# Kernel tuning notes

Hardware: AMD Instinct MI355X
Metric: run time of the kernel (lower is better)

## Reference

```python
import jax, jax.numpy as jnp
import numpy as np

EPSILON = 1e-09
BETA = 0.75  # original code clamps negative-sample sigmoid to min=BETA (reproduced faithfully)
B, D, V, NUM_SAMPLES = 262144, 256, 50000, 5


def setup_inputs() -> dict:
    key = jax.random.key(0)
    k1, k2, k3, k4 = jax.random.split(key, 4)
    context = jax.random.normal(k1, (B, D), dtype=jnp.float32)
    target = jax.random.normal(k2, (B, D), dtype=jnp.float32)
    emb = jax.random.normal(k3, (V, D), dtype=jnp.float32)
    neg_idx = jax.random.randint(k4, (NUM_SAMPLES,), 0, V)  # precomputed unigram-table draws
    return {"context": context, "target": target, "emb": emb, "neg_idx": neg_idx}


def reference(context, target, emb, neg_idx):
    # positive term: log(sigmoid(<c, t>).clamp(min=EPSILON))
    dots = jnp.sum(context * target, axis=-1)  # [B]
    log_targets = jnp.log(jnp.clip(jax.nn.sigmoid(dots), EPSILON, None))
    # negative samples: NUM_SAMPLES embedding rows shared across the batch
    samples = emb[neg_idx]  # [S, D]
    neg_dots = -jnp.einsum('bd,sd->bs', context, samples)  # [B, S]
    log_samples = jnp.log(jnp.clip(jax.nn.sigmoid(neg_dots), BETA, None)).sum(axis=-1)  # [B]
    return jnp.sum(log_targets + log_samples)
```

## Files before the change

kernel.cpp:

```cpp
#include <hip/hip_runtime.h>

static constexpr int B_ROWS  = 262144;
static constexpr int D       = 256;
static constexpr int NSAMP   = 5;
static constexpr int BLOCK   = 256;
static constexpr int NBLOCKS = 4096;
static constexpr int WPB     = BLOCK / 64;
static constexpr int GPW     = 16;

static constexpr float NEG_LN_EPS  = 20.723265836946411f;
static constexpr float NEG_LN_BETA = 0.28768207245178085f;

__device__ __forceinline__ float dot4(const float4 a, const float4 b) {
    return a.x * b.x + a.y * b.y + a.z * b.z + a.w * b.w;
}

__global__ __launch_bounds__(BLOCK) void sgns_main(
    const float* __restrict__ ctx, const float* __restrict__ tgt,
    const float* __restrict__ emb, const int* __restrict__ neg_idx,
    float* __restrict__ partials)
{
    __shared__ float smp[NSAMP][D];
    for (int i = threadIdx.x; i < NSAMP * D; i += BLOCK) {
        const int s = i >> 8, c = i & (D - 1);
        smp[s][c] = emb[(size_t)neg_idx[s] * D + c];
    }
    __syncthreads();

    const int lane = threadIdx.x & 63;
    const int wid  = threadIdx.x >> 6;
    const int sub  = lane & 3;
    const int grp  = lane >> 2;
    const int gwave  = blockIdx.x * WPB + wid;
    const int nwaves = NBLOCKS * WPB;

    float acc = 0.0f;
    for (int rbase = gwave * GPW; rbase < B_ROWS; rbase += nwaves * GPW) {
        const float* cp = ctx + (size_t)(rbase + grp) * D + sub * 4;
        const float* tp = tgt + (size_t)(rbase + grp) * D + sub * 4;

        float d0 = 0.f, d1 = 0.f, d2 = 0.f, d3 = 0.f, d4 = 0.f, d5 = 0.f;
#pragma unroll 8
        for (int m = 0; m < 16; ++m) {
            const float4 c4 = *reinterpret_cast<const float4*>(cp + m * 16);
            const float4 t4 = *reinterpret_cast<const float4*>(tp + m * 16);
            const int sc = m * 16 + sub * 4;
            const float4 s0 = *reinterpret_cast<const float4*>(&smp[0][sc]);
            const float4 s1 = *reinterpret_cast<const float4*>(&smp[1][sc]);
            const float4 s2 = *reinterpret_cast<const float4*>(&smp[2][sc]);
            const float4 s3 = *reinterpret_cast<const float4*>(&smp[3][sc]);
            const float4 s4 = *reinterpret_cast<const float4*>(&smp[4][sc]);
            d0 += dot4(c4, t4);
            d1 += dot4(c4, s0);
            d2 += dot4(c4, s1);
            d3 += dot4(c4, s2);
            d4 += dot4(c4, s3);
            d5 += dot4(c4, s4);
        }

        d0 += __shfl_xor(d0, 1, 64); d0 += __shfl_xor(d0, 2, 64);
        d1 += __shfl_xor(d1, 1, 64); d1 += __shfl_xor(d1, 2, 64);
        d2 += __shfl_xor(d2, 1, 64); d2 += __shfl_xor(d2, 2, 64);
        d3 += __shfl_xor(d3, 1, 64); d3 += __shfl_xor(d3, 2, 64);
        d4 += __shfl_xor(d4, 1, 64); d4 += __shfl_xor(d4, 2, 64);
        d5 += __shfl_xor(d5, 1, 64); d5 += __shfl_xor(d5, 2, 64);

        float row_loss = -fminf(__logf(1.0f + __expf(-d0)), NEG_LN_EPS);
        row_loss -= fminf(__logf(1.0f + __expf(d1)), NEG_LN_BETA);
        row_loss -= fminf(__logf(1.0f + __expf(d2)), NEG_LN_BETA);
        row_loss -= fminf(__logf(1.0f + __expf(d3)), NEG_LN_BETA);
        row_loss -= fminf(__logf(1.0f + __expf(d4)), NEG_LN_BETA);
        row_loss -= fminf(__logf(1.0f + __expf(d5)), NEG_LN_BETA);
        acc += row_loss;
    }

#pragma unroll
    for (int off = 32; off > 0; off >>= 1) acc += __shfl_xor(acc, off, 64);
    acc *= 0.25f;

    __shared__ float blk[WPB];
    if (lane == 0) blk[wid] = acc;
    __syncthreads();
    if (threadIdx.x == 0) {
        float s = 0.0f;
#pragma unroll
        for (int i = 0; i < WPB; ++i) s += blk[i];
        partials[blockIdx.x] = s;
    }
}

__global__ __launch_bounds__(256) void sgns_reduce(
    const float* __restrict__ partials, float* __restrict__ out)
{
    float s = 0.0f;
    for (int i = threadIdx.x; i < NBLOCKS; i += 256) s += partials[i];
#pragma unroll
    for (int off = 32; off > 0; off >>= 1) s += __shfl_xor(s, off, 64);
    __shared__ float lds[4];
    if ((threadIdx.x & 63) == 0) lds[threadIdx.x >> 6] = s;
    __syncthreads();
    if (threadIdx.x == 0) out[0] = lds[0] + lds[1] + lds[2] + lds[3];
}

extern "C" void kernel_launch(void* const* d_in, const int* in_sizes, int n_in,
                              void* d_out, int out_size, void* d_ws, size_t ws_size,
                              hipStream_t stream) {
    const float* ctx     = (const float*)d_in[0];
    const float* tgt     = (const float*)d_in[1];
    const float* emb     = (const float*)d_in[2];
    const int*   neg_idx = (const int*)d_in[3];
    float* out      = (float*)d_out;
    float* partials = (float*)d_ws;

    sgns_main<<<NBLOCKS, BLOCK, 0, stream>>>(ctx, tgt, emb, neg_idx, partials);
    sgns_reduce<<<1, 256, 0, stream>>>(partials, out);
}
```

Measured before the change: 110.7 us.

## Double-buffer context/target loads into LDS via async global_load_lds

Rewrites the main loop so each wave streams its rows in 32-column chunks through a double-buffered LDS staging area, using direct global-to-LDS loads, and waits on vmcnt so the next chunk's fetch overlaps the current chunk's math. The grid is halved so each wave handles exactly two row groups over a fully unrolled 16-step schedule. This aims to hide memory latency in a bandwidth-bound reduction, at the cost of hard-coding the row coverage to the grid size and adding LDS traffic and extra waitcnt stalls.

```diff
diff --git a/kernel.cpp b/kernel.cpp
--- a/kernel.cpp
+++ b/kernel.cpp
@@ -4,15 +4,33 @@
 static constexpr int D       = 256;
 static constexpr int NSAMP   = 5;
 static constexpr int BLOCK   = 256;
-static constexpr int NBLOCKS = 4096;
+static constexpr int NBLOCKS = 2048;
 static constexpr int WPB     = BLOCK / 64;
 static constexpr int GPW     = 16;
+static constexpr int CHUNK   = 32;
+static constexpr int NSTEP   = 16;
 
 static constexpr float NEG_LN_EPS  = 20.723265836946411f;
 static constexpr float NEG_LN_BETA = 0.28768207245178085f;
 
+typedef __attribute__((address_space(3))) void       lds_void;
+typedef const __attribute__((address_space(1))) void g_void;
+
 __device__ __forceinline__ float dot4(const float4 a, const float4 b) {
     return a.x * b.x + a.y * b.y + a.z * b.z + a.w * b.w;
+}
+
+__device__ __forceinline__ void issue_stage(
+    const float* __restrict__ ctx, const float* __restrict__ tgt,
+    float* sc_base, float* st_base, int rowbase, int col, int lane)
+{
+    const size_t off = (size_t)(rowbase + (lane >> 2)) * D + col + (lane & 3) * 4;
+    const float* gc = ctx + off;
+    const float* gt = tgt + off;
+    __builtin_amdgcn_global_load_lds((g_void*)(gc),      (lds_void*)(sc_base),       16, 0, 0);
+    __builtin_amdgcn_global_load_lds((g_void*)(gc + 16), (lds_void*)(sc_base + 256), 16, 0, 0);
+    __builtin_amdgcn_global_load_lds((g_void*)(gt),      (lds_void*)(st_base),       16, 0, 0);
+    __builtin_amdgcn_global_load_lds((g_void*)(gt + 16), (lds_void*)(st_base + 256), 16, 0, 0);
 }
 
 __global__ __launch_bounds__(BLOCK) void sgns_main(
@@ -21,6 +39,7 @@
     float* __restrict__ partials)
 {
     __shared__ float smp[NSAMP][D];
+    __shared__ float stage[WPB][2][2][2][16][16];
     for (int i = threadIdx.x; i < NSAMP * D; i += BLOCK) {
         const int s = i >> 8, c = i & (D - 1);
         smp[s][c] = emb[(size_t)neg_idx[s] * D + c];
@@ -33,18 +52,35 @@
     const int grp  = lane >> 2;
     const int gwave  = blockIdx.x * WPB + wid;
     const int nwaves = NBLOCKS * WPB;
+    const int r0 = gwave * GPW;
+    const int r1 = r0 + nwaves * GPW;
 
     float acc = 0.0f;
-    for (int rbase = gwave * GPW; rbase < B_ROWS; rbase += nwaves * GPW) {
-        const float* cp = ctx + (size_t)(rbase + grp) * D + sub * 4;
-        const float* tp = tgt + (size_t)(rbase + grp) * D + sub * 4;
+    float d0 = 0.f, d1 = 0.f, d2 = 0.f, d3 = 0.f, d4 = 0.f, d5 = 0.f;
 
-        float d0 = 0.f, d1 = 0.f, d2 = 0.f, d3 = 0.f, d4 = 0.f, d5 = 0.f;
-#pragma unroll 8
-        for (int m = 0; m < 16; ++m) {
-            const float4 c4 = *reinterpret_cast<const float4*>(cp + m * 16);
-            const float4 t4 = *reinterpret_cast<const float4*>(tp + m * 16);
-            const int sc = m * 16 + sub * 4;
+    issue_stage(ctx, tgt, &stage[wid][0][0][0][0][0], &stage[wid][0][1][0][0][0],
+                r0, 0, lane);
+
+#pragma unroll
+    for (int s = 0; s < NSTEP; ++s) {
+        const int b = s & 1;
+        if (s + 1 < NSTEP) {
+            const int rb  = ((s + 1) >= 8) ? r1 : r0;
+            const int ncol = ((s + 1) & 7) * CHUNK;
+            issue_stage(ctx, tgt, &stage[wid][b ^ 1][0][0][0][0],
+                        &stage[wid][b ^ 1][1][0][0][0], rb, ncol, lane);
+            asm volatile("s_waitcnt vmcnt(4)" ::: "memory");
+        } else {
+            asm volatile("s_waitcnt vmcnt(0)" ::: "memory");
+        }
+        __builtin_amdgcn_sched_barrier(0);
+
+        const int col = (s & 7) * CHUNK;
+#pragma unroll
+        for (int m = 0; m < 2; ++m) {
+            const float4 c4 = *reinterpret_cast<const float4*>(&stage[wid][b][0][m][grp][sub * 4]);
+            const float4 t4 = *reinterpret_cast<const float4*>(&stage[wid][b][1][m][grp][sub * 4]);
+            const int sc = col + m * 16 + sub * 4;
             const float4 s0 = *reinterpret_cast<const float4*>(&smp[0][sc]);
             const float4 s1 = *reinterpret_cast<const float4*>(&smp[1][sc]);
             const float4 s2 = *reinterpret_cast<const float4*>(&smp[2][sc]);
@@ -58,20 +94,23 @@
             d5 += dot4(c4, s4);
         }
 
-        d0 += __shfl_xor(d0, 1, 64); d0 += __shfl_xor(d0, 2, 64);
-        d1 += __shfl_xor(d1, 1, 64); d1 += __shfl_xor(d1, 2, 64);
-        d2 += __shfl_xor(d2, 1, 64); d2 += __shfl_xor(d2, 2, 64);
-        d3 += __shfl_xor(d3, 1, 64); d3 += __shfl_xor(d3, 2, 64);
-        d4 += __shfl_xor(d4, 1, 64); d4 += __shfl_xor(d4, 2, 64);
-        d5 += __shfl_xor(d5, 1, 64); d5 += __shfl_xor(d5, 2, 64);
+        if ((s & 7) == 7) {
+            d0 += __shfl_xor(d0, 1, 64); d0 += __shfl_xor(d0, 2, 64);
+            d1 += __shfl_xor(d1, 1, 64); d1 += __shfl_xor(d1, 2, 64);
+            d2 += __shfl_xor(d2, 1, 64); d2 += __shfl_xor(d2, 2, 64);
+            d3 += __shfl_xor(d3, 1, 64); d3 += __shfl_xor(d3, 2, 64);
+            d4 += __shfl_xor(d4, 1, 64); d4 += __shfl_xor(d4, 2, 64);
+            d5 += __shfl_xor(d5, 1, 64); d5 += __shfl_xor(d5, 2, 64);
 
-        float row_loss = -fminf(__logf(1.0f + __expf(-d0)), NEG_LN_EPS);
-        row_loss -= fminf(__logf(1.0f + __expf(d1)), NEG_LN_BETA);
-        row_loss -= fminf(__logf(1.0f + __expf(d2)), NEG_LN_BETA);
-        row_loss -= fminf(__logf(1.0f + __expf(d3)), NEG_LN_BETA);
-        row_loss -= fminf(__logf(1.0f + __expf(d4)), NEG_LN_BETA);
-        row_loss -= fminf(__logf(1.0f + __expf(d5)), NEG_LN_BETA);
-        acc += row_loss;
+            float row_loss = -fminf(__logf(1.0f + __expf(-d0)), NEG_LN_EPS);
+            row_loss -= fminf(__logf(1.0f + __expf(d1)), NEG_LN_BETA);
+            row_loss -= fminf(__logf(1.0f + __expf(d2)), NEG_LN_BETA);
+            row_loss -= fminf(__logf(1.0f + __expf(d3)), NEG_LN_BETA);
+            row_loss -= fminf(__logf(1.0f + __expf(d4)), NEG_LN_BETA);
+            row_loss -= fminf(__logf(1.0f + __expf(d5)), NEG_LN_BETA);
+            acc += row_loss;
+            d0 = d1 = d2 = d3 = d4 = d5 = 0.f;
+        }
     }
 
 #pragma unroll
```

Measured after the change: 100.1 us. -9.6%, faster.

## Double-buffer row loads into LDS with async global_load_lds per wave

Applied to the files above, without the earlier changes.

Each wave now streams context and target rows directly into a per-wave LDS double buffer using global_load_lds, four rows per step over eight steps. The next step's loads are issued before computing on the current buffer, with explicit vmcnt waits. Work is remapped so 16 lanes cooperate on each row, with a wider shuffle reduction. The grid is halved so each wave handles a fixed 32-row chunk. The aim is deeper memory-level parallelism on a bandwidth-bound stream. In exchange, the roughly 69KB of LDS per block limits occupancy, and the kernel now relies on gfx950 direct-to-LDS loads.

```diff
diff --git a/kernel.cpp b/kernel.cpp
--- a/kernel.cpp
+++ b/kernel.cpp
@@ -4,15 +4,32 @@
 static constexpr int D       = 256;
 static constexpr int NSAMP   = 5;
 static constexpr int BLOCK   = 256;
-static constexpr int NBLOCKS = 4096;
+static constexpr int NBLOCKS = 2048;
 static constexpr int WPB     = BLOCK / 64;
-static constexpr int GPW     = 16;
+static constexpr int RPS     = 4;
+static constexpr int NSTEP   = 8;
 
 static constexpr float NEG_LN_EPS  = 20.723265836946411f;
 static constexpr float NEG_LN_BETA = 0.28768207245178085f;
 
+typedef __attribute__((address_space(3))) void       lds_void;
+typedef const __attribute__((address_space(1))) void g_void;
+
 __device__ __forceinline__ float dot4(const float4 a, const float4 b) {
     return a.x * b.x + a.y * b.y + a.z * b.z + a.w * b.w;
+}
+
+__device__ __forceinline__ void issue_step(
+    const float* __restrict__ ctx, const float* __restrict__ tgt,
+    float* dst_c, float* dst_t, int rowbase, int lane)
+{
+#pragma unroll
+    for (int k = 0; k < RPS; ++k) {
+        const float* gc = ctx + (size_t)(rowbase + k) * D + lane * 4;
+        const float* gt = tgt + (size_t)(rowbase + k) * D + lane * 4;
+        __builtin_amdgcn_global_load_lds((g_void*)gc, (lds_void*)(dst_c + k * D), 16, 0, 0);
+        __builtin_amdgcn_global_load_lds((g_void*)gt, (lds_void*)(dst_t + k * D), 16, 0, 0);
+    }
 }
 
 __global__ __launch_bounds__(BLOCK) void sgns_main(
@@ -21,6 +38,7 @@
     float* __restrict__ partials)
 {
     __shared__ float smp[NSAMP][D];
+    __shared__ float stage[WPB][2][2][RPS][D];
     for (int i = threadIdx.x; i < NSAMP * D; i += BLOCK) {
         const int s = i >> 8, c = i & (D - 1);
         smp[s][c] = emb[(size_t)neg_idx[s] * D + c];
@@ -29,27 +47,38 @@
 
     const int lane = threadIdx.x & 63;
     const int wid  = threadIdx.x >> 6;
-    const int sub  = lane & 3;
-    const int grp  = lane >> 2;
-    const int gwave  = blockIdx.x * WPB + wid;
-    const int nwaves = NBLOCKS * WPB;
+    const int g4   = lane >> 4;
+    const int s16  = lane & 15;
+    const int gwave = blockIdx.x * WPB + wid;
+    const int R = gwave * (RPS * NSTEP);
 
     float acc = 0.0f;
-    for (int rbase = gwave * GPW; rbase < B_ROWS; rbase += nwaves * GPW) {
-        const float* cp = ctx + (size_t)(rbase + grp) * D + sub * 4;
-        const float* tp = tgt + (size_t)(rbase + grp) * D + sub * 4;
+
+    issue_step(ctx, tgt, &stage[wid][0][0][0][0], &stage[wid][0][1][0][0], R, lane);
+
+#pragma unroll
+    for (int s = 0; s < NSTEP; ++s) {
+        const int b = s & 1;
+        if (s + 1 < NSTEP) {
+            issue_step(ctx, tgt, &stage[wid][b ^ 1][0][0][0],
+                       &stage[wid][b ^ 1][1][0][0], R + (s + 1) * RPS, lane);
+            asm volatile("s_waitcnt vmcnt(8)" ::: "memory");
+        } else {
+            asm volatile("s_waitcnt vmcnt(0)" ::: "memory");
+        }
+        __builtin_amdgcn_sched_barrier(0);
 
         float d0 = 0.f, d1 = 0.f, d2 = 0.f, d3 = 0.f, d4 = 0.f, d5 = 0.f;
-#pragma unroll 8
-        for (int m = 0; m < 16; ++m) {
-            const float4 c4 = *reinterpret_cast<const float4*>(cp + m * 16);
-            const float4 t4 = *reinterpret_cast<const float4*>(tp + m * 16);
-            const int sc = m * 16 + sub * 4;
-            const float4 s0 = *reinterpret_cast<const float4*>(&smp[0][sc]);
-            const float4 s1 = *reinterpret_cast<const float4*>(&smp[1][sc]);
-            const float4 s2 = *reinterpret_cast<const float4*>(&smp[2][sc]);
-            const float4 s3 = *reinterpret_cast<const float4*>(&smp[3][sc]);
-            const float4 s4 = *reinterpret_cast<const float4*>(&smp[4][sc]);
+#pragma unroll
+        for (int m = 0; m < 4; ++m) {
+            const int gw = (m * 16 + s16) * 4;
+            const float4 c4 = *reinterpret_cast<const float4*>(&stage[wid][b][0][g4][gw]);
+            const float4 t4 = *reinterpret_cast<const float4*>(&stage[wid][b][1][g4][gw]);
+            const float4 s0 = *reinterpret_cast<const float4*>(&smp[0][gw]);
+            const float4 s1 = *reinterpret_cast<const float4*>(&smp[1][gw]);
+            const float4 s2 = *reinterpret_cast<const float4*>(&smp[2][gw]);
+            const float4 s3 = *reinterpret_cast<const float4*>(&smp[3][gw]);
+            const float4 s4 = *reinterpret_cast<const float4*>(&smp[4][gw]);
             d0 += dot4(c4, t4);
             d1 += dot4(c4, s0);
             d2 += dot4(c4, s1);
@@ -58,12 +87,15 @@
             d5 += dot4(c4, s4);
         }
 
-        d0 += __shfl_xor(d0, 1, 64); d0 += __shfl_xor(d0, 2, 64);
-        d1 += __shfl_xor(d1, 1, 64); d1 += __shfl_xor(d1, 2, 64);
-        d2 += __shfl_xor(d2, 1, 64); d2 += __shfl_xor(d2, 2, 64);
-        d3 += __shfl_xor(d3, 1, 64); d3 += __shfl_xor(d3, 2, 64);
-        d4 += __shfl_xor(d4, 1, 64); d4 += __shfl_xor(d4, 2, 64);
-        d5 += __shfl_xor(d5, 1, 64); d5 += __shfl_xor(d5, 2, 64);
+#pragma unroll
+        for (int off = 1; off < 16; off <<= 1) {
+            d0 += __shfl_xor(d0, off, 64);
+            d1 += __shfl_xor(d1, off, 64);
+            d2 += __shfl_xor(d2, off, 64);
+            d3 += __shfl_xor(d3, off, 64);
+            d4 += __shfl_xor(d4, off, 64);
+            d5 += __shfl_xor(d5, off, 64);
+        }
 
         float row_loss = -fminf(__logf(1.0f + __expf(-d0)), NEG_LN_EPS);
         row_loss -= fminf(__logf(1.0f + __expf(d1)), NEG_LN_BETA);
@@ -74,9 +106,8 @@
         acc += row_loss;
     }
 
-#pragma unroll
-    for (int off = 32; off > 0; off >>= 1) acc += __shfl_xor(acc, off, 64);
-    acc *= 0.25f;
+    acc += __shfl_xor(acc, 16, 64);
+    acc += __shfl_xor(acc, 32, 64);
 
     __shared__ float blk[WPB];
     if (lane == 0) blk[wid] = acc;
```

After: 106.4 us. 3.9% less time.

## Fuse final reduction into main kernel via last-block atomic counter

Applied to the files above, without the earlier changes.

Replaces the separate single-block reduction kernel with a last-block-done pattern: each block publishes its partial with a release store, bumps an atomic counter, and the final block sums all partials and writes the output. This removes one kernel launch and its gap, at the cost of a memset per call. The grid is also halved so each wave processes more rows, and the inner loop unroll is reduced, which changes memory-level parallelism and register pressure.

```diff
diff --git a/kernel.cpp b/kernel.cpp
--- a/kernel.cpp
+++ b/kernel.cpp
@@ -4,7 +4,7 @@
 static constexpr int D       = 256;
 static constexpr int NSAMP   = 5;
 static constexpr int BLOCK   = 256;
-static constexpr int NBLOCKS = 4096;
+static constexpr int NBLOCKS = 2048;
 static constexpr int WPB     = BLOCK / 64;
 static constexpr int GPW     = 16;
 
@@ -18,7 +18,8 @@
 __global__ __launch_bounds__(BLOCK) void sgns_main(
     const float* __restrict__ ctx, const float* __restrict__ tgt,
     const float* __restrict__ emb, const int* __restrict__ neg_idx,
-    float* __restrict__ partials)
+    float* __restrict__ partials, unsigned int* __restrict__ counter,
+    float* __restrict__ out)
 {
     __shared__ float smp[NSAMP][D];
     for (int i = threadIdx.x; i < NSAMP * D; i += BLOCK) {
@@ -40,7 +41,7 @@
         const float* tp = tgt + (size_t)(rbase + grp) * D + sub * 4;
 
         float d0 = 0.f, d1 = 0.f, d2 = 0.f, d3 = 0.f, d4 = 0.f, d5 = 0.f;
-#pragma unroll 8
+#pragma unroll 4
         for (int m = 0; m < 16; ++m) {
             const float4 c4 = *reinterpret_cast<const float4*>(cp + m * 16);
             const float4 t4 = *reinterpret_cast<const float4*>(tp + m * 16);
@@ -81,25 +82,37 @@
     __shared__ float blk[WPB];
     if (lane == 0) blk[wid] = acc;
     __syncthreads();
+
+    __shared__ int last_flag;
     if (threadIdx.x == 0) {
         float s = 0.0f;
 #pragma unroll
         for (int i = 0; i < WPB; ++i) s += blk[i];
-        partials[blockIdx.x] = s;
+        __hip_atomic_store(&partials[blockIdx.x], s, __ATOMIC_RELEASE,
+                           __HIP_MEMORY_SCOPE_AGENT);
+        const unsigned int old = __hip_atomic_fetch_add(
+            counter, 1u, __ATOMIC_ACQ_REL, __HIP_MEMORY_SCOPE_AGENT);
+        last_flag = (old == (unsigned int)(NBLOCKS - 1));
     }
-}
+    __syncthreads();
 
-__global__ __launch_bounds__(256) void sgns_reduce(
-    const float* __restrict__ partials, float* __restrict__ out)
-{
-    float s = 0.0f;
-    for (int i = threadIdx.x; i < NBLOCKS; i += 256) s += partials[i];
+    if (last_flag) {
+        float t = 0.0f;
+        for (int i = threadIdx.x; i < NBLOCKS; i += BLOCK)
+            t += __hip_atomic_load(&partials[i], __ATOMIC_RELAXED,
+                                   __HIP_MEMORY_SCOPE_AGENT);
 #pragma unroll
-    for (int off = 32; off > 0; off >>= 1) s += __shfl_xor(s, off, 64);
-    __shared__ float lds[4];
-    if ((threadIdx.x & 63) == 0) lds[threadIdx.x >> 6] = s;
-    __syncthreads();
-    if (threadIdx.x == 0) out[0] = lds[0] + lds[1] + lds[2] + lds[3];
+        for (int off = 32; off > 0; off >>= 1) t += __shfl_xor(t, off, 64);
+        __shared__ float fin[WPB];
+        if (lane == 0) fin[wid] = t;
+        __syncthreads();
+        if (threadIdx.x == 0) {
+            float s = 0.0f;
+#pragma unroll
+            for (int i = 0; i < WPB; ++i) s += fin[i];
+            out[0] = s;
+        }
+    }
 }
 
 extern "C" void kernel_launch(void* const* d_in, const int* in_sizes, int n_in,
@@ -111,7 +124,10 @@
     const int*   neg_idx = (const int*)d_in[3];
     float* out      = (float*)d_out;
     float* partials = (float*)d_ws;
+    unsigned int* counter = (unsigned int*)((char*)d_ws + NBLOCKS * sizeof(float));
 
-    sgns_main<<<NBLOCKS, BLOCK, 0, stream>>>(ctx, tgt, emb, neg_idx, partials);
-    sgns_reduce<<<1, 256, 0, stream>>>(partials, out);
+    hipMemsetAsync(counter, 0, sizeof(unsigned int), stream);
+
+    sgns_main<<<NBLOCKS, BLOCK, 0, stream>>>(ctx, tgt, emb, neg_idx,
+                                             partials, counter, out);
 }
```

Result: slower. 276.2 us (+149.5%).
